# Performance work log

Hardware: AMD Instinct MI355X
Metric: run time of the kernel (lower is better)

Reference implementation:

```python
import jax, jax.numpy as jnp
import numpy as np

IN_F, OUT_F, RANK = 4096, 4096, 64
B, S = 4, 2048


def setup_inputs() -> dict:
    key = jax.random.key(0)
    k1, k2, k3 = jax.random.split(key, 3)
    x = jax.random.normal(k1, (B, S, IN_F), dtype=jnp.float32)
    # Low-rank compressed weight factors: W = U @ V^T, shape [OUT_F, IN_F]
    U = jax.random.normal(k2, (OUT_F, RANK), dtype=jnp.float32) / np.sqrt(RANK)
    V = jax.random.normal(k3, (IN_F, RANK), dtype=jnp.float32) / np.sqrt(IN_F)
    bias = jnp.zeros((OUT_F,), dtype=jnp.float32)
    return {"x": x, "U": U, "V": V, "bias": bias}


def reference(x, U, V, bias):
    # Decompress: weight = compressor.decompress(compressed_weight) -> [out, in]
    weight = jnp.einsum("or,ir->oi", U, V)  # materialized like the original
    # F.linear(x, weight, bias) = x @ weight^T + bias
    return jnp.einsum("bsi,oi->bso", x, weight) + bias
```

## Files before the change

### kernel.cpp

```cpp
#include <hip/hip_runtime.h>

#define IN_F    4096
#define OUT_F   4096
#define RANK    64
#define M_TOTAL 8192
#define M_TILE  16
#define BLOCK   512
#define NWAVES  8
#define KSPLIT  4

using short8  = __attribute__((ext_vector_type(8))) short;
using float4v = __attribute__((ext_vector_type(4))) float;

#define MFMA16(A, B, C) __builtin_amdgcn_mfma_f32_16x16x32_bf16((A), (B), (C), 0, 0, 0)

__device__ __forceinline__ void split2(float x, short& h, short& l) {
    unsigned u = __float_as_uint(x);
    unsigned t = u & 0xffff0000u;
    h = (short)(t >> 16);
    float r = x - __uint_as_float(t);
    l = (short)(__float_as_uint(r) >> 16);
}

__device__ __forceinline__ void split_f4x2(float4 a, float4 b, short8& hi, short8& lo) {
    short h0,h1,h2,h3,h4,h5,h6,h7, l0,l1,l2,l3,l4,l5,l6,l7;
    split2(a.x,h0,l0); split2(a.y,h1,l1); split2(a.z,h2,l2); split2(a.w,h3,l3);
    split2(b.x,h4,l4); split2(b.y,h5,l5); split2(b.z,h6,l6); split2(b.w,h7,l7);
    hi = (short8){h0,h1,h2,h3,h4,h5,h6,h7};
    lo = (short8){l0,l1,l2,l3,l4,l5,l6,l7};
}


__global__ void prep_uv(const float* __restrict__ V, const float* __restrict__ U,
                        unsigned short* __restrict__ vt_hi, unsigned short* __restrict__ vt_lo,
                        unsigned short* __restrict__ u_hi,  unsigned short* __restrict__ u_lo)
{
    const int b = blockIdx.x;
    const int linear = (b & 255) * 256 + threadIdx.x;
    short h[4], l[4];
    if (b < 256) {
        const int r  = linear >> 10;
        const int k0 = (linear & 1023) * 4;
        #pragma unroll
        for (int i = 0; i < 4; ++i)
            split2(V[(size_t)(k0 + i) * RANK + r], h[i], l[i]);
        const size_t o = (size_t)r * IN_F + k0;
        *(ushort4*)(vt_hi + o) = make_ushort4((unsigned short)h[0], (unsigned short)h[1],
                                              (unsigned short)h[2], (unsigned short)h[3]);
        *(ushort4*)(vt_lo + o) = make_ushort4((unsigned short)l[0], (unsigned short)l[1],
                                              (unsigned short)l[2], (unsigned short)l[3]);
    } else {
        const int idx = linear * 4;
        const float4 u4 = *(const float4*)(U + idx);
        split2(u4.x, h[0], l[0]); split2(u4.y, h[1], l[1]);
        split2(u4.z, h[2], l[2]); split2(u4.w, h[3], l[3]);
        *(ushort4*)(u_hi + idx) = make_ushort4((unsigned short)h[0], (unsigned short)h[1],
                                               (unsigned short)h[2], (unsigned short)h[3]);
        *(ushort4*)(u_lo + idx) = make_ushort4((unsigned short)l[0], (unsigned short)l[1],
                                               (unsigned short)l[2], (unsigned short)l[3]);
    }
}

__global__ __launch_bounds__(512, 4) void lowrank_xv5(
    const float* __restrict__ x,
    const unsigned short* __restrict__ vt_hi, const unsigned short* __restrict__ vt_lo,
    float* __restrict__ t_part)
{
    __shared__ float          xs[2][64][36];
    __shared__ unsigned short vs[2][2][64][40];

    const int tid  = threadIdx.x;
    const int wv   = tid >> 6;
    const int lane = tid & 63;
    const int l15  = lane & 15;
    const int quad = lane >> 4;
    const int msub = wv >> 1;
    const int rsub = wv & 1;
    const int kq   = blockIdx.x & 3;
    const int mg   = blockIdx.x >> 2;
    const int m0   = mg * 64;
    const int kbase = kq * 1024;

    const int sxr = tid >> 3, sxc = (tid & 7) * 4;
    const int svp = tid >> 8;
    const int svr = (tid & 255) >> 2, svc = (tid & 3) * 8;
    const float*          xg = x + (size_t)(m0 + sxr) * IN_F + kbase + sxc;
    const unsigned short* vg = (svp ? vt_lo : vt_hi) + (size_t)svr * IN_F + kbase + svc;

    {
        float4 x0 = *(const float4*)(xg);
        short8 v0 = *(const short8*)(vg);
        *(float4*)(&xs[0][sxr][sxc]) = x0;
        *(short8*)(&vs[0][svp][svr][svc]) = v0;
    }
    __syncthreads();

    float4v acc[2] = {};
    for (int ks = 0; ks < 32; ++ks) {
        const int cur = ks & 1;
        float4 nx = {0.f, 0.f, 0.f, 0.f};
        short8 nv = {};
        if (ks < 31) {
            nx = *(const float4*)(xg + (ks + 1) * 32);
            nv = *(const short8*)(vg + (ks + 1) * 32);
        }
        float4 xa = *(const float4*)(&xs[cur][msub * 16 + l15][quad * 8]);
        float4 xb = *(const float4*)(&xs[cur][msub * 16 + l15][quad * 8 + 4]);
        short8 a_hi, a_lo;
        split_f4x2(xa, xb, a_hi, a_lo);
        #pragma unroll
        for (int rt = 0; rt < 2; ++rt) {
            const int rr = rsub * 32 + rt * 16 + l15;
            short8 bhv = *(const short8*)(&vs[cur][0][rr][quad * 8]);
            short8 blv = *(const short8*)(&vs[cur][1][rr][quad * 8]);
            acc[rt] = MFMA16(a_lo, bhv, acc[rt]);
            acc[rt] = MFMA16(a_hi, blv, acc[rt]);
            acc[rt] = MFMA16(a_hi, bhv, acc[rt]);
        }
        if (ks < 31) {
            *(float4*)(&xs[cur ^ 1][sxr][sxc]) = nx;
            *(short8*)(&vs[cur ^ 1][svp][svr][svc]) = nv;
        }
        __syncthreads();
    }

    float* base = t_part + (size_t)kq * (M_TOTAL * RANK);
    #pragma unroll
    for (int rt = 0; rt < 2; ++rt)
        #pragma unroll
        for (int rg = 0; rg < 4; ++rg)
            base[(size_t)(m0 + msub * 16 + quad * 4 + rg) * RANK
                 + rsub * 32 + rt * 16 + l15] = acc[rt][rg];
}

__global__ __launch_bounds__(256, 4) void lowrank_tu5(
    const float* __restrict__ t_part,
    const unsigned short* __restrict__ u_hi, const unsigned short* __restrict__ u_lo,
    const float* __restrict__ bias, float* __restrict__ out)
{
    const int tid  = threadIdx.x;
    const int wv   = tid >> 6;
    const int lane = tid & 63;
    const int l15  = lane & 15;
    const int quad = lane >> 4;
    const int og   = blockIdx.x & 31;
    const int mg   = blockIdx.x >> 5;
    const int m0   = mg * 128 + wv * 32;
    const int o0   = og * 128;

    short8 ta_hi[2][2], ta_lo[2][2];
    #pragma unroll
    for (int mf = 0; mf < 2; ++mf) {
        const float* tp = t_part + (size_t)(m0 + mf * 16 + l15) * RANK + quad * 8;
        float4 s0 = *(const float4*)(tp);
        float4 s1 = *(const float4*)(tp + 4);
        float4 s2 = *(const float4*)(tp + 32);
        float4 s3 = *(const float4*)(tp + 36);
        #pragma unroll
        for (int p = 1; p < KSPLIT; ++p) {
            const float* q = tp + (size_t)p * (M_TOTAL * RANK);
            const float4 a0 = *(const float4*)(q);
            const float4 a1 = *(const float4*)(q + 4);
            const float4 a2 = *(const float4*)(q + 32);
            const float4 a3 = *(const float4*)(q + 36);
            s0.x += a0.x; s0.y += a0.y; s0.z += a0.z; s0.w += a0.w;
            s1.x += a1.x; s1.y += a1.y; s1.z += a1.z; s1.w += a1.w;
            s2.x += a2.x; s2.y += a2.y; s2.z += a2.z; s2.w += a2.w;
            s3.x += a3.x; s3.y += a3.y; s3.z += a3.z; s3.w += a3.w;
        }
        split_f4x2(s0, s1, ta_hi[mf][0], ta_lo[mf][0]);
        split_f4x2(s2, s3, ta_hi[mf][1], ta_lo[mf][1]);
    }

    const unsigned short* up_h = u_hi + (size_t)(o0 + l15) * RANK + quad * 8;
    const unsigned short* up_l = u_lo + (size_t)(o0 + l15) * RANK + quad * 8;
    short8 uh0 = *(const short8*)(up_h), uh1 = *(const short8*)(up_h + 32);
    short8 ul0 = *(const short8*)(up_l), ul1 = *(const short8*)(up_l + 32);

    #pragma unroll
    for (int nt = 0; nt < 8; ++nt) {
        short8 nh0 = uh0, nh1 = uh1, nl0 = ul0, nl1 = ul1;
        if (nt < 7) {
            const int adv = (nt + 1) * 16 * RANK;
            nh0 = *(const short8*)(up_h + adv);   nh1 = *(const short8*)(up_h + adv + 32);
            nl0 = *(const short8*)(up_l + adv);   nl1 = *(const short8*)(up_l + adv + 32);
        }
        const int o = o0 + nt * 16 + l15;
        const float bv = bias[o];
        #pragma unroll
        for (int mf = 0; mf < 2; ++mf) {
            float4v acc = {bv, bv, bv, bv};
            acc = MFMA16(ta_lo[mf][0], uh0, acc);
            acc = MFMA16(ta_hi[mf][0], ul0, acc);
            acc = MFMA16(ta_hi[mf][0], uh0, acc);
            acc = MFMA16(ta_lo[mf][1], uh1, acc);
            acc = MFMA16(ta_hi[mf][1], ul1, acc);
            acc = MFMA16(ta_hi[mf][1], uh1, acc);
            float* op = out + (size_t)(m0 + mf * 16 + quad * 4) * OUT_F + o;
            op[0 * OUT_F] = acc[0];
            op[1 * OUT_F] = acc[1];
            op[2 * OUT_F] = acc[2];
            op[3 * OUT_F] = acc[3];
        }
        uh0 = nh0; uh1 = nh1; ul0 = nl0; ul1 = nl1;
    }
}


__global__ __launch_bounds__(BLOCK, 4) void lowrank_xv(
    const float* __restrict__ x,
    const unsigned short* __restrict__ vt_hi, const unsigned short* __restrict__ vt_lo,
    unsigned short* __restrict__ t_hi, unsigned short* __restrict__ t_lo)
{
    __shared__ float part[NWAVES][M_TILE][RANK + 4];

    const int tid  = threadIdx.x;
    const int wv   = tid >> 6;
    const int lane = tid & 63;
    const int l15  = lane & 15;
    const int quad = lane >> 4;
    const int m0   = blockIdx.x * M_TILE;

    float4v acc[4] = {};
    const float*          xp = x     + (size_t)(m0 + l15) * IN_F + wv * 512 + quad * 8;
    const unsigned short* vh = vt_hi + (size_t)l15 * IN_F + wv * 512 + quad * 8;
    const unsigned short* vl = vt_lo + (size_t)l15 * IN_F + wv * 512 + quad * 8;

    float4 xa = *(const float4*)(xp);
    float4 xb = *(const float4*)(xp + 4);
    #pragma unroll
    for (int ks = 0; ks < 16; ++ks) {
        const int k0 = ks * 32;
        float4 na = xa, nb = xb;
        if (ks < 15) {
            na = *(const float4*)(xp + k0 + 32);
            nb = *(const float4*)(xp + k0 + 36);
        }
        short8 a_hi, a_lo;
        split_f4x2(xa, xb, a_hi, a_lo);
        #pragma unroll
        for (int rt = 0; rt < 4; ++rt) {
            short8 b_hi = *(const short8*)(vh + (size_t)rt * 16 * IN_F + k0);
            short8 b_lo = *(const short8*)(vl + (size_t)rt * 16 * IN_F + k0);
            acc[rt] = MFMA16(a_lo, b_hi, acc[rt]);
            acc[rt] = MFMA16(a_hi, b_lo, acc[rt]);
            acc[rt] = MFMA16(a_hi, b_hi, acc[rt]);
        }
        xa = na; xb = nb;
    }

    #pragma unroll
    for (int rt = 0; rt < 4; ++rt)
        #pragma unroll
        for (int rg = 0; rg < 4; ++rg)
            part[wv][quad * 4 + rg][rt * 16 + l15] = acc[rt][rg];
    __syncthreads();

    const int e = tid * 2;
    const int m = e >> 6, r = e & 63;
    float s0 = 0.f, s1 = 0.f;
    #pragma unroll
    for (int w = 0; w < NWAVES; ++w) { s0 += part[w][m][r]; s1 += part[w][m][r + 1]; }
    short h0, l0, h1, l1;
    split2(s0, h0, l0); split2(s1, h1, l1);
    const size_t off = (size_t)m0 * RANK + e;
    *(ushort2*)(t_hi + off) = make_ushort2((unsigned short)h0, (unsigned short)h1);
    *(ushort2*)(t_lo + off) = make_ushort2((unsigned short)l0, (unsigned short)l1);
}

__global__ __launch_bounds__(256, 4) void lowrank_tu(
    const unsigned short* __restrict__ t_hi, const unsigned short* __restrict__ t_lo,
    const unsigned short* __restrict__ u_hi, const unsigned short* __restrict__ u_lo,
    const float* __restrict__ bias, float* __restrict__ out)
{
    const int tid  = threadIdx.x;
    const int wv   = tid >> 6;
    const int lane = tid & 63;
    const int l15  = lane & 15;
    const int quad = lane >> 4;
    const int og   = blockIdx.x & 7;
    const int mg   = blockIdx.x >> 3;
    const int m0   = mg * 64 + wv * 16;
    const int o0   = og * 512;

    short8 ta_hi[2], ta_lo[2];
    {
        const unsigned short* tp_h = t_hi + (size_t)(m0 + l15) * RANK + quad * 8;
        const unsigned short* tp_l = t_lo + (size_t)(m0 + l15) * RANK + quad * 8;
        ta_hi[0] = *(const short8*)(tp_h);   ta_hi[1] = *(const short8*)(tp_h + 32);
        ta_lo[0] = *(const short8*)(tp_l);   ta_lo[1] = *(const short8*)(tp_l + 32);
    }

    #pragma unroll 2
    for (int nt = 0; nt < 32; ++nt) {
        const int o = o0 + nt * 16 + l15;
        const unsigned short* up_h = u_hi + (size_t)o * RANK + quad * 8;
        const unsigned short* up_l = u_lo + (size_t)o * RANK + quad * 8;
        const float bv = bias[o];
        float4v acc = {bv, bv, bv, bv};
        #pragma unroll
        for (int ks = 0; ks < 2; ++ks) {
            short8 uh = *(const short8*)(up_h + ks * 32);
            short8 ul = *(const short8*)(up_l + ks * 32);
            acc = MFMA16(ta_lo[ks], uh, acc);
            acc = MFMA16(ta_hi[ks], ul, acc);
            acc = MFMA16(ta_hi[ks], uh, acc);
        }
        float* op = out + (size_t)(m0 + quad * 4) * OUT_F + o;
        op[0 * OUT_F] = acc[0];
        op[1 * OUT_F] = acc[1];
        op[2 * OUT_F] = acc[2];
        op[3 * OUT_F] = acc[3];
    }
}

__global__ __launch_bounds__(256, 2) void fallback_fp32(
    const float* __restrict__ x, const float* __restrict__ U,
    const float* __restrict__ V, const float* __restrict__ bias,
    float* __restrict__ out)
{
    __shared__ float v_lds[128][RANK];
    __shared__ float t_lds[8][RANK];
    const int tid = threadIdx.x, lane = tid & 63, wave = tid >> 6;
    const int m0 = blockIdx.x * 8;
    float acc0 = 0.f, acc1 = 0.f;
    const size_t row_base = (size_t)(m0 + wave * 2) * IN_F;
    for (int kt = 0; kt < IN_F; kt += 128) {
        const float4* Vg = (const float4*)(V + (size_t)kt * RANK);
        float4* Vs = (float4*)(&v_lds[0][0]);
        #pragma unroll
        for (int i = 0; i < 8; ++i) Vs[tid + 256 * i] = Vg[tid + 256 * i];
        __syncthreads();
        const float* xp = x + row_base + kt;
        #pragma unroll 8
        for (int k = 0; k < 128; k += 4) {
            float v0 = v_lds[k+0][lane], v1 = v_lds[k+1][lane];
            float v2 = v_lds[k+2][lane], v3 = v_lds[k+3][lane];
            float4 xa = *(const float4*)(xp + 0 * IN_F + k);
            float4 xb = *(const float4*)(xp + 1 * IN_F + k);
            acc0 += xa.x*v0 + xa.y*v1 + xa.z*v2 + xa.w*v3;
            acc1 += xb.x*v0 + xb.y*v1 + xb.z*v2 + xb.w*v3;
        }
        __syncthreads();
    }
    t_lds[wave*2+0][lane] = acc0;
    t_lds[wave*2+1][lane] = acc1;
    __syncthreads();
    for (int oc = 0; oc < OUT_F; oc += 1024) {
        const int o4 = oc + tid * 4;
        const float4 b4 = *(const float4*)(bias + o4);
        float4 a0=b4,a1=b4,a2=b4,a3=b4,a4=b4,a5=b4,a6=b4,a7=b4;
        const float* Up = U + (size_t)o4 * RANK;
        #pragma unroll 2
        for (int r0 = 0; r0 < RANK; r0 += 4) {
            const float4 u0 = *(const float4*)(Up + 0*RANK + r0);
            const float4 u1 = *(const float4*)(Up + 1*RANK + r0);
            const float4 u2 = *(const float4*)(Up + 2*RANK + r0);
            const float4 u3 = *(const float4*)(Up + 3*RANK + r0);
            #define P2_STEP(AM, MM) { \
                const float4 t4 = *(const float4*)(&t_lds[MM][r0]); \
                AM.x += t4.x*u0.x + t4.y*u0.y + t4.z*u0.z + t4.w*u0.w; \
                AM.y += t4.x*u1.x + t4.y*u1.y + t4.z*u1.z + t4.w*u1.w; \
                AM.z += t4.x*u2.x + t4.y*u2.y + t4.z*u2.z + t4.w*u2.w; \
                AM.w += t4.x*u3.x + t4.y*u3.y + t4.z*u3.z + t4.w*u3.w; }
            P2_STEP(a0,0) P2_STEP(a1,1) P2_STEP(a2,2) P2_STEP(a3,3)
            P2_STEP(a4,4) P2_STEP(a5,5) P2_STEP(a6,6) P2_STEP(a7,7)
            #undef P2_STEP
        }
        float* op = out + (size_t)m0 * OUT_F + o4;
        *(float4*)(op+0*OUT_F)=a0; *(float4*)(op+1*OUT_F)=a1;
        *(float4*)(op+2*OUT_F)=a2; *(float4*)(op+3*OUT_F)=a3;
        *(float4*)(op+4*OUT_F)=a4; *(float4*)(op+5*OUT_F)=a5;
        *(float4*)(op+6*OUT_F)=a6; *(float4*)(op+7*OUT_F)=a7;
    }
}

extern "C" void kernel_launch(void* const* d_in, const int* in_sizes, int n_in,
                              void* d_out, int out_size, void* d_ws, size_t ws_size,
                              hipStream_t stream) {
    const float* x    = (const float*)d_in[0];
    const float* U    = (const float*)d_in[1];
    const float* V    = (const float*)d_in[2];
    const float* bias = (const float*)d_in[3];
    float* out = (float*)d_out;

    const size_t E = (size_t)RANK * IN_F;
    const size_t T = (size_t)M_TOTAL * RANK;
    const size_t need_v6 = (E * 4) * sizeof(unsigned short)
                         + (size_t)KSPLIT * T * sizeof(float);
    const size_t need_v2 = (E * 4 + T * 2) * sizeof(unsigned short);

    if (ws_size >= need_v6) {
        unsigned short* vt_hi = (unsigned short*)d_ws;
        unsigned short* vt_lo = vt_hi + E;
        unsigned short* u_hi  = vt_lo + E;
        unsigned short* u_lo  = u_hi  + E;
        float*          t_part = (float*)(u_lo + E);
        prep_uv<<<dim3(512), dim3(256), 0, stream>>>(V, U, vt_hi, vt_lo, u_hi, u_lo);
        lowrank_xv5<<<dim3((M_TOTAL / 64) * KSPLIT), dim3(512), 0, stream>>>(
            x, vt_hi, vt_lo, t_part);
        lowrank_tu5<<<dim3((M_TOTAL / 128) * (OUT_F / 128)), dim3(256), 0, stream>>>(
            t_part, u_hi, u_lo, bias, out);
    } else if (ws_size >= need_v2) {
        unsigned short* vt_hi = (unsigned short*)d_ws;
        unsigned short* vt_lo = vt_hi + E;
        unsigned short* u_hi  = vt_lo + E;
        unsigned short* u_lo  = u_hi  + E;
        unsigned short* t_hi  = u_lo  + E;
        unsigned short* t_lo  = t_hi  + T;
        prep_uv<<<dim3(512), dim3(256), 0, stream>>>(V, U, vt_hi, vt_lo, u_hi, u_lo);
        lowrank_xv<<<dim3(M_TOTAL / M_TILE), dim3(BLOCK), 0, stream>>>(
            x, vt_hi, vt_lo, t_hi, t_lo);
        lowrank_tu<<<dim3((M_TOTAL / 64) * (OUT_F / 512)), dim3(256), 0, stream>>>(
            t_hi, t_lo, u_hi, u_lo, bias, out);
    } else {
        fallback_fp32<<<dim3(M_TOTAL / 8), dim3(256), 0, stream>>>(x, U, V, bias, out);
    }
}
```

Baseline: 303.5 us.

## Halve xv M-tile to double blocks and transpose tu MFMA for vectorized stores

The x·V kernel now uses 32-row M tiles with 8 waves each covering 16 rank columns. This doubles the grid size for more parallelism, but each V tile staged in shared memory is reused across half as many rows. The T·U kernel swaps the MFMA operand order so each lane holds 4 consecutive output columns, which allows float4 stores of the output and a float4 bias load in place of 4 strided scalar stores. The main goal is to cut the cost of writing the large output tensor through better store coalescing.

```diff
diff --git a/kernel.cpp b/kernel.cpp
--- a/kernel.cpp
+++ b/kernel.cpp
@@ -61,12 +61,12 @@
     }
 }
 
-__global__ __launch_bounds__(512, 4) void lowrank_xv5(
+__global__ __launch_bounds__(512, 4) void lowrank_xv6(
     const float* __restrict__ x,
     const unsigned short* __restrict__ vt_hi, const unsigned short* __restrict__ vt_lo,
     float* __restrict__ t_part)
 {
-    __shared__ float          xs[2][64][36];
+    __shared__ float          xs[2][32][36];
     __shared__ unsigned short vs[2][2][64][40];
 
     const int tid  = threadIdx.x;
@@ -74,11 +74,11 @@
     const int lane = tid & 63;
     const int l15  = lane & 15;
     const int quad = lane >> 4;
-    const int msub = wv >> 1;
-    const int rsub = wv & 1;
+    const int msub = wv >> 2;
+    const int rsub = wv & 3;
     const int kq   = blockIdx.x & 3;
     const int mg   = blockIdx.x >> 2;
-    const int m0   = mg * 64;
+    const int m0   = mg * 32;
     const int kbase = kq * 1024;
 
     const int sxr = tid >> 3, sxc = (tid & 7) * 4;
@@ -88,37 +88,38 @@
     const unsigned short* vg = (svp ? vt_lo : vt_hi) + (size_t)svr * IN_F + kbase + svc;
 
     {
-        float4 x0 = *(const float4*)(xg);
         short8 v0 = *(const short8*)(vg);
-        *(float4*)(&xs[0][sxr][sxc]) = x0;
+        if (tid < 256) {
+            float4 x0 = *(const float4*)(xg);
+            *(float4*)(&xs[0][sxr][sxc]) = x0;
+        }
         *(short8*)(&vs[0][svp][svr][svc]) = v0;
     }
     __syncthreads();
 
-    float4v acc[2] = {};
+    float4v acc = {};
     for (int ks = 0; ks < 32; ++ks) {
         const int cur = ks & 1;
         float4 nx = {0.f, 0.f, 0.f, 0.f};
         short8 nv = {};
         if (ks < 31) {
-            nx = *(const float4*)(xg + (ks + 1) * 32);
+            if (tid < 256) nx = *(const float4*)(xg + (ks + 1) * 32);
             nv = *(const short8*)(vg + (ks + 1) * 32);
         }
         float4 xa = *(const float4*)(&xs[cur][msub * 16 + l15][quad * 8]);
         float4 xb = *(const float4*)(&xs[cur][msub * 16 + l15][quad * 8 + 4]);
         short8 a_hi, a_lo;
         split_f4x2(xa, xb, a_hi, a_lo);
-        #pragma unroll
-        for (int rt = 0; rt < 2; ++rt) {
-            const int rr = rsub * 32 + rt * 16 + l15;
+        {
+            const int rr = rsub * 16 + l15;
             short8 bhv = *(const short8*)(&vs[cur][0][rr][quad * 8]);
             short8 blv = *(const short8*)(&vs[cur][1][rr][quad * 8]);
-            acc[rt] = MFMA16(a_lo, bhv, acc[rt]);
-            acc[rt] = MFMA16(a_hi, blv, acc[rt]);
-            acc[rt] = MFMA16(a_hi, bhv, acc[rt]);
+            acc = MFMA16(a_lo, bhv, acc);
+            acc = MFMA16(a_hi, blv, acc);
+            acc = MFMA16(a_hi, bhv, acc);
         }
         if (ks < 31) {
-            *(float4*)(&xs[cur ^ 1][sxr][sxc]) = nx;
+            if (tid < 256) *(float4*)(&xs[cur ^ 1][sxr][sxc]) = nx;
             *(short8*)(&vs[cur ^ 1][svp][svr][svc]) = nv;
         }
         __syncthreads();
@@ -126,14 +127,12 @@
 
     float* base = t_part + (size_t)kq * (M_TOTAL * RANK);
     #pragma unroll
-    for (int rt = 0; rt < 2; ++rt)
-        #pragma unroll
-        for (int rg = 0; rg < 4; ++rg)
-            base[(size_t)(m0 + msub * 16 + quad * 4 + rg) * RANK
-                 + rsub * 32 + rt * 16 + l15] = acc[rt][rg];
-}
-
-__global__ __launch_bounds__(256, 4) void lowrank_tu5(
+    for (int rg = 0; rg < 4; ++rg)
+        base[(size_t)(m0 + msub * 16 + quad * 4 + rg) * RANK
+             + rsub * 16 + l15] = acc[rg];
+}
+
+__global__ __launch_bounds__(256, 4) void lowrank_tu6(
     const float* __restrict__ t_part,
     const unsigned short* __restrict__ u_hi, const unsigned short* __restrict__ u_lo,
     const float* __restrict__ bias, float* __restrict__ out)
@@ -148,7 +147,7 @@
     const int m0   = mg * 128 + wv * 32;
     const int o0   = og * 128;
 
-    short8 ta_hi[2][2], ta_lo[2][2];
+    short8 tb_hi[2][2], tb_lo[2][2];
     #pragma unroll
     for (int mf = 0; mf < 2; ++mf) {
         const float* tp = t_part + (size_t)(m0 + mf * 16 + l15) * RANK + quad * 8;
@@ -168,8 +167,8 @@
             s2.x += a2.x; s2.y += a2.y; s2.z += a2.z; s2.w += a2.w;
             s3.x += a3.x; s3.y += a3.y; s3.z += a3.z; s3.w += a3.w;
         }
-        split_f4x2(s0, s1, ta_hi[mf][0], ta_lo[mf][0]);
-        split_f4x2(s2, s3, ta_hi[mf][1], ta_lo[mf][1]);
+        split_f4x2(s0, s1, tb_hi[mf][0], tb_lo[mf][0]);
+        split_f4x2(s2, s3, tb_hi[mf][1], tb_lo[mf][1]);
     }
 
     const unsigned short* up_h = u_hi + (size_t)(o0 + l15) * RANK + quad * 8;
@@ -185,22 +184,19 @@
             nh0 = *(const short8*)(up_h + adv);   nh1 = *(const short8*)(up_h + adv + 32);
             nl0 = *(const short8*)(up_l + adv);   nl1 = *(const short8*)(up_l + adv + 32);
         }
-        const int o = o0 + nt * 16 + l15;
-        const float bv = bias[o];
+        const int oc = o0 + nt * 16;
+        const float4 bv4 = *(const float4*)(bias + oc + quad * 4);
         #pragma unroll
         for (int mf = 0; mf < 2; ++mf) {
-            float4v acc = {bv, bv, bv, bv};
-            acc = MFMA16(ta_lo[mf][0], uh0, acc);
-            acc = MFMA16(ta_hi[mf][0], ul0, acc);
-            acc = MFMA16(ta_hi[mf][0], uh0, acc);
-            acc = MFMA16(ta_lo[mf][1], uh1, acc);
-            acc = MFMA16(ta_hi[mf][1], ul1, acc);
-            acc = MFMA16(ta_hi[mf][1], uh1, acc);
-            float* op = out + (size_t)(m0 + mf * 16 + quad * 4) * OUT_F + o;
-            op[0 * OUT_F] = acc[0];
-            op[1 * OUT_F] = acc[1];
-            op[2 * OUT_F] = acc[2];
-            op[3 * OUT_F] = acc[3];
+            float4v acc = {bv4.x, bv4.y, bv4.z, bv4.w};
+            acc = MFMA16(uh0, tb_lo[mf][0], acc);
+            acc = MFMA16(ul0, tb_hi[mf][0], acc);
+            acc = MFMA16(uh0, tb_hi[mf][0], acc);
+            acc = MFMA16(uh1, tb_lo[mf][1], acc);
+            acc = MFMA16(ul1, tb_hi[mf][1], acc);
+            acc = MFMA16(uh1, tb_hi[mf][1], acc);
+            float4 v = {acc[0], acc[1], acc[2], acc[3]};
+            *(float4*)(out + (size_t)(m0 + mf * 16 + l15) * OUT_F + oc + quad * 4) = v;
         }
         uh0 = nh0; uh1 = nh1; ul0 = nl0; ul1 = nl1;
     }
@@ -386,20 +382,20 @@
 
     const size_t E = (size_t)RANK * IN_F;
     const size_t T = (size_t)M_TOTAL * RANK;
-    const size_t need_v6 = (E * 4) * sizeof(unsigned short)
+    const size_t need_v7 = (E * 4) * sizeof(unsigned short)
                          + (size_t)KSPLIT * T * sizeof(float);
     const size_t need_v2 = (E * 4 + T * 2) * sizeof(unsigned short);
 
-    if (ws_size >= need_v6) {
+    if (ws_size >= need_v7) {
         unsigned short* vt_hi = (unsigned short*)d_ws;
         unsigned short* vt_lo = vt_hi + E;
         unsigned short* u_hi  = vt_lo + E;
         unsigned short* u_lo  = u_hi  + E;
         float*          t_part = (float*)(u_lo + E);
         prep_uv<<<dim3(512), dim3(256), 0, stream>>>(V, U, vt_hi, vt_lo, u_hi, u_lo);
-        lowrank_xv5<<<dim3((M_TOTAL / 64) * KSPLIT), dim3(512), 0, stream>>>(
+        lowrank_xv6<<<dim3((M_TOTAL / 32) * KSPLIT), dim3(512), 0, stream>>>(
             x, vt_hi, vt_lo, t_part);
-        lowrank_tu5<<<dim3((M_TOTAL / 128) * (OUT_F / 128)), dim3(256), 0, stream>>>(
+        lowrank_tu6<<<dim3((M_TOTAL / 128) * (OUT_F / 128)), dim3(256), 0, stream>>>(
             t_part, u_hi, u_lo, bias, out);
     } else if (ws_size >= need_v2) {
         unsigned short* vt_hi = (unsigned short*)d_ws;
```

Result: slower. 322.9 us (+6.4%).
